# Performance work log

Hardware: AMD Instinct MI355X
Metric: run time of the kernel (lower is better)

The kernel has to match this reference:

```python
import jax, jax.numpy as jnp
import numpy as np

_EPS = 1e-6

def _qmul(q1, q2):  # xyzw quaternion product
    x1, y1, z1, w1 = q1[..., 0], q1[..., 1], q1[..., 2], q1[..., 3]
    x2, y2, z2, w2 = q2[..., 0], q2[..., 1], q2[..., 2], q2[..., 3]
    return jnp.stack([
        w1 * x2 + x1 * w2 + y1 * z2 - z1 * y2,
        w1 * y2 + y1 * w2 + z1 * x2 - x1 * z2,
        w1 * z2 + z1 * w2 + x1 * y2 - y1 * x2,
        w1 * w2 - x1 * x2 - y1 * y2 - z1 * z2], axis=-1)

def _qrot(q, v):  # rotate v by unit quaternion q (xyzw)
    qv, qw = q[..., :3], q[..., 3:4]
    t = 2.0 * jnp.cross(qv, v)
    return v + qw * t + jnp.cross(qv, t)

def _so3_log(q):  # quaternion (xyzw) -> rotation vector phi
    qv, qw = q[..., :3], q[..., 3:4]
    n2 = jnp.sum(qv * qv, axis=-1, keepdims=True)
    small = n2 < _EPS * _EPS
    n = jnp.sqrt(jnp.where(small, 1.0, n2))
    factor = jnp.where(small,
                       2.0 / qw - (2.0 / 3.0) * n2 / qw ** 3,
                       2.0 * jnp.arctan2(n, qw) / n)
    return factor * qv

def _so3_exp(phi):  # rotation vector -> quaternion (xyzw)
    t2 = jnp.sum(phi * phi, axis=-1, keepdims=True)
    small = t2 < _EPS * _EPS
    theta = jnp.sqrt(jnp.where(small, 1.0, t2))
    half = 0.5 * theta
    s = jnp.where(small, 0.5 - t2 / 48.0, jnp.sin(half) / theta)
    w = jnp.where(small, 1.0 - t2 / 8.0, jnp.cos(half))
    return jnp.concatenate([s * phi, w], axis=-1)

def _jl(phi, v):  # SO3 left Jacobian J_l(phi) @ v
    t2 = jnp.sum(phi * phi, axis=-1, keepdims=True)
    small = t2 < _EPS * _EPS
    t2s = jnp.where(small, 1.0, t2)
    theta = jnp.sqrt(t2s)
    a = jnp.where(small, 0.5 - t2 / 24.0, (1.0 - jnp.cos(theta)) / t2s)
    b = jnp.where(small, 1.0 / 6.0 - t2 / 120.0, (theta - jnp.sin(theta)) / (t2s * theta))
    c1 = jnp.cross(phi, v)
    return v + a * c1 + b * jnp.cross(phi, c1)

def _jl_inv(phi, v):  # SO3 left Jacobian inverse J_l^{-1}(phi) @ v
    t2 = jnp.sum(phi * phi, axis=-1, keepdims=True)
    small = t2 < _EPS * _EPS
    t2s = jnp.where(small, 1.0, t2)
    theta = jnp.sqrt(t2s)
    s = jnp.sin(theta)
    s_safe = jnp.where(jnp.abs(s) < _EPS, _EPS, s)
    c = jnp.where(small, 1.0 / 12.0 + t2 / 720.0,
                  1.0 / t2s - (1.0 + jnp.cos(theta)) / (2.0 * theta * s_safe))
    c1 = jnp.cross(phi, v)
    return v - 0.5 * c1 + c * jnp.cross(phi, c1)

def _se3_inv(T):
    t, q = T[..., :3], T[..., 3:]
    qi = q * jnp.array([-1.0, -1.0, -1.0, 1.0], dtype=T.dtype)
    return jnp.concatenate([-_qrot(qi, t), qi], axis=-1)

def _se3_mul(T1, T2):
    t1, q1 = T1[..., :3], T1[..., 3:]
    t2, q2 = T2[..., :3], T2[..., 3:]
    return jnp.concatenate([t1 + _qrot(q1, t2), _qmul(q1, q2)], axis=-1)

def _se3_log(T):  # SE3 -> se3 [tau, phi]
    t, q = T[..., :3], T[..., 3:]
    phi = _so3_log(q)
    return jnp.concatenate([_jl_inv(phi, t), phi], axis=-1)

def _se3_exp(xi):  # se3 [tau, phi] -> SE3
    tau, phi = xi[..., :3], xi[..., 3:]
    q = _so3_exp(phi)
    return jnp.concatenate([_jl(phi, tau), q], axis=-1)

def _forward(input_poses, time):
    # duplicate first/last pose (inter_begin_and_end=True)
    poses = jnp.concatenate([input_poses[:, :1], input_poses, input_poses[:, -1:]], axis=1)
    B, P = poses.shape[0], poses.shape[1]
    S = P - 3  # number of spline segments
    u = time.reshape(-1)  # [K]
    K = u.shape[0]
    U = jnp.stack([jnp.ones_like(u), u, u * u, u * u * u], axis=0)  # [4,K]
    M = jnp.array([[5., 3., -3., 1.], [1., 3., 3., -2.], [0., 0., 0., 1.]], dtype=u.dtype) / 6.0
    w = M @ U  # [3,K] cumulative B-spline weights
    p0, p1 = poses[:, 0:S], poses[:, 1:S + 1]
    p2, p3 = poses[:, 2:S + 2], poses[:, 3:S + 3]
    d0 = _se3_log(_se3_mul(_se3_inv(p0), p1))  # [B,S,6]
    d1 = _se3_log(_se3_mul(_se3_inv(p1), p2))
    d2 = _se3_log(_se3_mul(_se3_inv(p2), p3))
    A0 = _se3_exp(d0[:, :, None, :] * w[0][None, None, :, None])  # [B,S,K,7]
    A1 = _se3_exp(d1[:, :, None, :] * w[1][None, None, :, None])
    A2 = _se3_exp(d2[:, :, None, :] * w[2][None, None, :, None])
    Td = jnp.broadcast_to(p0[:, :, None, :], (B, S, K, 7))
    out = _se3_mul(_se3_mul(_se3_mul(Td, A0), A1), A2)
    return out.reshape(B, S * K, 7)

def setup_inputs() -> dict:
    key = jax.random.key(0)
    k1, k2, k3 = jax.random.split(key, 3)
    B, N, K = 32, 2048, 32
    t = jax.random.normal(k1, (B, N, 3), dtype=jnp.float32) * 2.0
    q = jax.random.normal(k2, (B, N, 4), dtype=jnp.float32)
    q = q / jnp.linalg.norm(q, axis=-1, keepdims=True)
    q = jnp.where(q[..., 3:4] < 0, -q, q)  # qw >= 0 for well-conditioned Log
    input_poses = jnp.concatenate([t, q], axis=-1)
    time = jax.random.uniform(k3, (1, 1, K), dtype=jnp.float32)
    return {"input_poses": input_poses, "time": time}

def reference(input_poses, time):
    return _forward(input_poses, time)
```

## Files before the change

### kernel.cpp

```cpp
#include <hip/hip_runtime.h>
#include <cmath>

namespace {

constexpr int BATCH  = 32;
constexpr int NPOSE  = 2048;
constexpr int KSAMP  = 32;
constexpr int NSEG   = NPOSE - 1;
constexpr int NDELTA = NPOSE + 1;
constexpr int SEGB   = 8;
constexpr float EPS  = 1e-6f;
constexpr float EPS2 = 1e-12f;
constexpr float INV_TWO_PI = 0.15915494309189535f;

struct V3 { float x, y, z; };
struct Q4 { float x, y, z, w; };
struct SE3 { V3 t; Q4 q; };

__device__ __forceinline__ float frcp(float x)  { return __builtin_amdgcn_rcpf(x); }
__device__ __forceinline__ float fsqrt(float x) { return __builtin_amdgcn_sqrtf(x); }
__device__ __forceinline__ float fsin(float x)  { return __builtin_amdgcn_sinf(x * INV_TWO_PI); }
__device__ __forceinline__ float fcos(float x)  { return __builtin_amdgcn_cosf(x * INV_TWO_PI); }

__device__ __forceinline__ V3 v3add(V3 a, V3 b) { return {a.x + b.x, a.y + b.y, a.z + b.z}; }
__device__ __forceinline__ V3 v3sub(V3 a, V3 b) { return {a.x - b.x, a.y - b.y, a.z - b.z}; }
__device__ __forceinline__ V3 v3scl(V3 a, float s) { return {a.x * s, a.y * s, a.z * s}; }
__device__ __forceinline__ float v3dot(V3 a, V3 b) { return a.x * b.x + a.y * b.y + a.z * b.z; }
__device__ __forceinline__ V3 v3cross(V3 a, V3 b) {
    return {a.y * b.z - a.z * b.y, a.z * b.x - a.x * b.z, a.x * b.y - a.y * b.x};
}

__device__ __forceinline__ V3 qrot(Q4 q, V3 v) {
    V3 qv{q.x, q.y, q.z};
    V3 t = v3scl(v3cross(qv, v), 2.0f);
    return v3add(v3add(v, v3scl(t, q.w)), v3cross(qv, t));
}

__device__ __forceinline__ Q4 qmul(Q4 a, Q4 b) {
    return {a.w * b.x + a.x * b.w + a.y * b.z - a.z * b.y,
            a.w * b.y + a.y * b.w + a.z * b.x - a.x * b.z,
            a.w * b.z + a.z * b.w + a.x * b.y - a.y * b.x,
            a.w * b.w - a.x * b.x - a.y * b.y - a.z * b.z};
}

__device__ __forceinline__ SE3 se3_mul(SE3 A, SE3 Bv) {
    SE3 r;
    r.t = v3add(A.t, qrot(A.q, Bv.t));
    r.q = qmul(A.q, Bv.q);
    return r;
}

__device__ __forceinline__ float facos(float x) {
    float ax = fabsf(x);
    float p = -0.0012624911f;
    p = p * ax + 0.0066700901f;
    p = p * ax - 0.0170881256f;
    p = p * ax + 0.0308918810f;
    p = p * ax - 0.0501743046f;
    p = p * ax + 0.0889789874f;
    p = p * ax - 0.2145988016f;
    p = p * ax + 1.5707963050f;
    float r = fsqrt(fmaxf(1.0f - ax, 0.0f)) * p;
    return (x >= 0.0f) ? r : (3.14159265358979f - r);
}

__device__ __forceinline__ V3 so3_log(Q4 q) {
    V3 qv{q.x, q.y, q.z};
    float n2 = v3dot(qv, qv);
    bool small = n2 < EPS2;
    float n = fsqrt(small ? 1.0f : n2);
    float iw = frcp(q.w);
    float f_small = 2.0f * iw - (2.0f / 3.0f) * n2 * iw * iw * iw;
    float wc = fminf(fmaxf(q.w, -1.0f), 1.0f);
    float f_big = 2.0f * facos(wc) * frcp(n);
    return v3scl(qv, small ? f_small : f_big);
}

__device__ __forceinline__ V3 jl_inv(V3 phi, V3 v) {
    float t2 = v3dot(phi, phi);
    bool small = t2 < EPS2;
    float t2s = small ? 1.0f : t2;
    float theta = fsqrt(t2s);
    float s = fsin(theta), cth = fcos(theta);
    float s_safe = (fabsf(s) < EPS) ? EPS : s;
    float c_big = frcp(t2s) - (1.0f + cth) * frcp(2.0f * theta * s_safe);
    float c = small ? (1.0f / 12.0f + t2 * (1.0f / 720.0f)) : c_big;
    V3 c1 = v3cross(phi, v);
    return v3add(v3sub(v, v3scl(c1, 0.5f)), v3scl(v3cross(phi, c1), c));
}

__global__ __launch_bounds__(256) void lie_delta_kernel(
    const float* __restrict__ poses,
    float4* __restrict__ ws)
{
    const int i = blockIdx.x * 256 + threadIdx.x;
    const int b = blockIdx.y;
    if (i >= NDELTA) return;

    int ia = max(i - 1, 0);
    int ib = min(i, NPOSE - 1);
    const float* Pa = poses + ((size_t)b * NPOSE + ia) * 7;
    const float* Pb = poses + ((size_t)b * NPOSE + ib) * 7;
    V3 ta{Pa[0], Pa[1], Pa[2]}; Q4 qa{Pa[3], Pa[4], Pa[5], Pa[6]};
    V3 tb{Pb[0], Pb[1], Pb[2]}; Q4 qb{Pb[3], Pb[4], Pb[5], Pb[6]};

    Q4 qi{-qa.x, -qa.y, -qa.z, qa.w};
    V3 trel = qrot(qi, v3sub(tb, ta));
    Q4 qrel = qmul(qi, qb);
    V3 phi = so3_log(qrel);
    V3 tau = jl_inv(phi, trel);

    float n2 = v3dot(phi, phi);
    float nphi = fsqrt(n2);
    float inv_n = frcp(fmaxf(nphi, 1e-20f));
    V3 u  = v3scl(phi, inv_n);
    V3 c1 = v3cross(u, tau);
    V3 c2 = v3cross(u, c1);

    float4* row = ws + ((size_t)b * NDELTA + i) * 4;
    row[0] = make_float4(tau.x, tau.y, tau.z, nphi);
    row[1] = make_float4(u.x,  u.y,  u.z,  0.0f);
    row[2] = make_float4(c1.x, c1.y, c1.z, 0.0f);
    row[3] = make_float4(c2.x, c2.y, c2.z, 0.0f);
}

__device__ __forceinline__ SE3 exp_fast(float4 A, float4 U, float4 C1, float4 C2, float w) {
    float th = fmaxf(w * A.w, 1e-12f);
    float sh = fsin(0.5f * th), ch = fcos(0.5f * th);
    float it = frcp(th);
    float sA = 2.0f * sh * sh * it;
    float sB = 1.0f - 2.0f * sh * ch * it;
    SE3 r;
    r.q = {sh * U.x, sh * U.y, sh * U.z, ch};
    r.t = {w * (A.x + sA * C1.x + sB * C2.x),
           w * (A.y + sA * C1.y + sB * C2.y),
           w * (A.z + sA * C1.z + sB * C2.z)};
    return r;
}

__global__ __launch_bounds__(256) void lie_spline_kernel(
    const float* __restrict__ poses,
    const float* __restrict__ timev,
    const float4* __restrict__ ws,
    float* __restrict__ out)
{
    __shared__ float4 sdel[(SEGB + 2) * 4];
    __shared__ float  sp[SEGB * 8];
    __shared__ __align__(16) float stage[SEGB * KSAMP * 7];

    const int b   = blockIdx.y;
    const int s0  = blockIdx.x * SEGB;
    const int tid = threadIdx.x;

    {
        int nrow4 = min(SEGB + 2, NDELTA - s0) * 4;
        if (tid < nrow4)
            sdel[tid] = ws[((size_t)b * NDELTA + s0) * 4 + tid];
        else if (tid >= 64 && tid < 64 + SEGB * 7) {
            int j = tid - 64;
            int jseg = j / 7, jf = j - jseg * 7;
            int ip = max(s0 + jseg - 1, 0);
            sp[jseg * 8 + jf] = poses[((size_t)b * NPOSE + ip) * 7 + jf];
        }
    }
    __syncthreads();

    const int lane = tid & (KSAMP - 1);
    const int seg  = tid >> 5;
    const int s    = s0 + seg;

    if (s < NSEG) {
        float u  = timev[lane];
        float u2 = u * u, u3 = u2 * u;
        const float c6 = 1.0f / 6.0f;
        float w0 = (5.0f + 3.0f * u - 3.0f * u2 + u3) * c6;
        float w1 = (1.0f + 3.0f * u + 3.0f * u2 - 2.0f * u3) * c6;
        float w2 = u3 * c6;

        const float* P0 = sp + seg * 8;
        SE3 T{{P0[0], P0[1], P0[2]}, {P0[3], P0[4], P0[5], P0[6]}};

        const float4* r0 = sdel + seg * 4;
        T = se3_mul(T, exp_fast(r0[0], r0[1], r0[2],  r0[3],  w0));
        T = se3_mul(T, exp_fast(r0[4], r0[5], r0[6],  r0[7],  w1));
        T = se3_mul(T, exp_fast(r0[8], r0[9], r0[10], r0[11], w2));

        float* st = stage + (size_t)tid * 7;
        st[0] = T.t.x; st[1] = T.t.y; st[2] = T.t.z;
        st[3] = T.q.x; st[4] = T.q.y; st[5] = T.q.z; st[6] = T.q.w;
    }
    __syncthreads();

    int nseg_blk = min(NSEG - s0, SEGB);
    int nvec = nseg_blk * (KSAMP * 7 / 4);
    const float4* sv = reinterpret_cast<const float4*>(stage);
    float4* ov = reinterpret_cast<float4*>(out + ((size_t)b * NSEG + s0) * (size_t)(KSAMP * 7));
    for (int j = tid; j < nvec; j += 256) ov[j] = sv[j];
}

}

extern "C" void kernel_launch(void* const* d_in, const int* in_sizes, int n_in,
                              void* d_out, int out_size, void* d_ws, size_t ws_size,
                              hipStream_t stream) {
    const float* poses = (const float*)d_in[0];
    const float* timev = (const float*)d_in[1];
    float* out = (float*)d_out;
    float4* ws = (float4*)d_ws;
    (void)in_sizes; (void)n_in; (void)out_size; (void)ws_size;

    dim3 g1((NDELTA + 255) / 256, BATCH);
    lie_delta_kernel<<<g1, 256, 0, stream>>>(poses, ws);

    dim3 g2((NSEG + SEGB - 1) / SEGB, BATCH);
    lie_spline_kernel<<<g2, 256, 0, stream>>>(poses, timev, ws, out);
}
```

Before: 89.67 us.

## Compute four samples per thread and store directly to global without LDS staging

The spline kernel now gives each block 32 segments, and each thread computes 4 consecutive samples of one segment. Delta rows are held in registers across those samples and written out as 7 contiguous float4 stores, replacing the shared-memory staging buffer and its extra barrier. Spline weights are precomputed once per block into shared memory. This cuts the block count and the LDS round trip, but each thread's 112-byte stores are strided across lanes, so coalescing may be worse, and register pressure rises.

```diff
diff --git a/kernel.cpp b/kernel.cpp
--- a/kernel.cpp
+++ b/kernel.cpp
@@ -8,7 +8,7 @@
 constexpr int KSAMP  = 32;
 constexpr int NSEG   = NPOSE - 1;
 constexpr int NDELTA = NPOSE + 1;
-constexpr int SEGB   = 8;
+constexpr int SEGB   = 32;
 constexpr float EPS  = 1e-6f;
 constexpr float EPS2 = 1e-12f;
 constexpr float INV_TWO_PI = 0.15915494309189535f;
@@ -144,58 +144,68 @@
     const float4* __restrict__ ws,
     float* __restrict__ out)
 {
-    __shared__ float4 sdel[(SEGB + 2) * 4];
+    __shared__ float4 sdel[(SEGB + 2) * 5];
     __shared__ float  sp[SEGB * 8];
-    __shared__ __align__(16) float stage[SEGB * KSAMP * 7];
+    __shared__ float  sw[3 * KSAMP];
 
     const int b   = blockIdx.y;
     const int s0  = blockIdx.x * SEGB;
     const int tid = threadIdx.x;
 
-    {
-        int nrow4 = min(SEGB + 2, NDELTA - s0) * 4;
-        if (tid < nrow4)
-            sdel[tid] = ws[((size_t)b * NDELTA + s0) * 4 + tid];
-        else if (tid >= 64 && tid < 64 + SEGB * 7) {
-            int j = tid - 64;
-            int jseg = j / 7, jf = j - jseg * 7;
-            int ip = max(s0 + jseg - 1, 0);
-            sp[jseg * 8 + jf] = poses[((size_t)b * NPOSE + ip) * 7 + jf];
-        }
-    }
-    __syncthreads();
-
-    const int lane = tid & (KSAMP - 1);
-    const int seg  = tid >> 5;
-    const int s    = s0 + seg;
-
-    if (s < NSEG) {
-        float u  = timev[lane];
+    if (tid < (SEGB + 2) * 4) {
+        int row = tid >> 2, r = tid & 3;
+        int idx = min(s0 + row, NDELTA - 1);
+        sdel[row * 5 + r] = ws[((size_t)b * NDELTA + idx) * 4 + r];
+    }
+    if (tid < SEGB * 7) {
+        int jseg = tid / 7, c = tid - jseg * 7;
+        int ip = min(max(s0 + jseg - 1, 0), NPOSE - 1);
+        sp[jseg * 8 + c] = poses[((size_t)b * NPOSE + ip) * 7 + c];
+    }
+    if (tid >= 224) {
+        int l = tid - 224;
+        float u = timev[l];
         float u2 = u * u, u3 = u2 * u;
         const float c6 = 1.0f / 6.0f;
-        float w0 = (5.0f + 3.0f * u - 3.0f * u2 + u3) * c6;
-        float w1 = (1.0f + 3.0f * u + 3.0f * u2 - 2.0f * u3) * c6;
-        float w2 = u3 * c6;
-
-        const float* P0 = sp + seg * 8;
-        SE3 T{{P0[0], P0[1], P0[2]}, {P0[3], P0[4], P0[5], P0[6]}};
-
-        const float4* r0 = sdel + seg * 4;
-        T = se3_mul(T, exp_fast(r0[0], r0[1], r0[2],  r0[3],  w0));
-        T = se3_mul(T, exp_fast(r0[4], r0[5], r0[6],  r0[7],  w1));
-        T = se3_mul(T, exp_fast(r0[8], r0[9], r0[10], r0[11], w2));
-
-        float* st = stage + (size_t)tid * 7;
-        st[0] = T.t.x; st[1] = T.t.y; st[2] = T.t.z;
-        st[3] = T.q.x; st[4] = T.q.y; st[5] = T.q.z; st[6] = T.q.w;
+        sw[l]             = (5.0f + 3.0f * u - 3.0f * u2 + u3) * c6;
+        sw[KSAMP + l]     = (1.0f + 3.0f * u + 3.0f * u2 - 2.0f * u3) * c6;
+        sw[2 * KSAMP + l] = u3 * c6;
     }
     __syncthreads();
 
-    int nseg_blk = min(NSEG - s0, SEGB);
-    int nvec = nseg_blk * (KSAMP * 7 / 4);
-    const float4* sv = reinterpret_cast<const float4*>(stage);
-    float4* ov = reinterpret_cast<float4*>(out + ((size_t)b * NSEG + s0) * (size_t)(KSAMP * 7));
-    for (int j = tid; j < nvec; j += 256) ov[j] = sv[j];
+    const int segl = tid >> 3;
+    const int s    = s0 + segl;
+    if (s >= NSEG) return;
+    const int k0   = (tid & 7) * 4;
+
+    const float4* R0 = sdel + segl * 5;
+    const float4* R1 = R0 + 5;
+    const float4* R2 = R0 + 10;
+    float4 A0 = R0[0], U0 = R0[1], C10 = R0[2], C20 = R0[3];
+    float4 A1 = R1[0], U1 = R1[1], C11 = R1[2], C21 = R1[3];
+    float4 A2 = R2[0], U2 = R2[1], C12 = R2[2], C22 = R2[3];
+
+    const float* P0 = sp + segl * 8;
+    const SE3 Tp{{P0[0], P0[1], P0[2]}, {P0[3], P0[4], P0[5], P0[6]}};
+
+    float buf[4 * 7];
+    #pragma unroll
+    for (int j = 0; j < 4; ++j) {
+        int k = k0 + j;
+        float w0 = sw[k], w1 = sw[KSAMP + k], w2 = sw[2 * KSAMP + k];
+        SE3 T = se3_mul(Tp, exp_fast(A0, U0, C10, C20, w0));
+        T = se3_mul(T, exp_fast(A1, U1, C11, C21, w1));
+        T = se3_mul(T, exp_fast(A2, U2, C12, C22, w2));
+        float* d = buf + j * 7;
+        d[0] = T.t.x; d[1] = T.t.y; d[2] = T.t.z;
+        d[3] = T.q.x; d[4] = T.q.y; d[5] = T.q.z; d[6] = T.q.w;
+    }
+
+    float4* ov = reinterpret_cast<float4*>(
+        out + ((size_t)b * NSEG + s0) * (size_t)(KSAMP * 7) + (size_t)tid * 28);
+    #pragma unroll
+    for (int c = 0; c < 7; ++c)
+        ov[c] = make_float4(buf[4 * c], buf[4 * c + 1], buf[4 * c + 2], buf[4 * c + 3]);
 }
 
 }
```

New measurement: 95.44 us. 1.06x slower.
